# Kernel tuning notes

Hardware: AMD Instinct MI355X
Metric: run time of the kernel (lower is better)

## Reference

```python
import jax, jax.numpy as jnp
import numpy as np

B, S, D, H = 2, 2048, 1024, 16
HD = D // H


def setup_inputs() -> dict:
    key = jax.random.key(0)
    ks = jax.random.split(key, 9)
    s = 1.0 / np.sqrt(D)
    return {
        "qx": jax.random.normal(ks[0], (B, S, D), jnp.float32),
        "kx": jax.random.normal(ks[1], (B, S, D), jnp.float32),
        "vx": jax.random.normal(ks[2], (B, S, D), jnp.float32),
        "mask": jnp.tril(jnp.ones((S, S), jnp.int32))[None, None],  # [1,1,S,S] causal
        "Wq": jax.random.uniform(ks[3], (D, D), jnp.float32, -s, s),
        "bq": jax.random.uniform(ks[4], (D,), jnp.float32, -s, s),
        "Wk": jax.random.uniform(ks[5], (D, D), jnp.float32, -s, s),
        "bk": jax.random.uniform(ks[6], (D,), jnp.float32, -s, s),
        "Wv": jax.random.uniform(ks[7], (D, D), jnp.float32, -s, s),
        "bv": jax.random.uniform(ks[8], (D,), jnp.float32, -s, s),
    }


def reference(qx, kx, vx, mask, Wq, bq, Wk, bk, Wv, bv):
    bat, seq_len, d_model = qx.shape
    # torch Linear: y = x @ W.T + b
    q = qx @ Wq.T + bq
    k = kx @ Wk.T + bk
    v = vx @ Wv.T + bv
    # [b, h, s, hd]
    q = q.reshape(bat, seq_len, H, HD).transpose(0, 2, 1, 3)
    k = k.reshape(bat, seq_len, H, HD).transpose(0, 2, 1, 3)
    v = v.reshape(bat, seq_len, H, HD).transpose(0, 2, 1, 3)
    # NOTE: original scales by sqrt(d_model), not sqrt(head_dim)
    attn_weight = jnp.einsum('bhqd,bhkd->bhqk', q, k) / jnp.sqrt(
        jnp.asarray(d_model, q.dtype))
    attn_weight = jnp.where(mask == 0, -jnp.inf, attn_weight)
    attn_score = jax.nn.softmax(attn_weight, axis=-1)
    attn_output = jnp.einsum('bhqk,bhkd->bhqd', attn_score, v)
    return attn_output.transpose(0, 2, 1, 3).reshape(bat, seq_len, d_model)
```

## Files before the change

kernel.cpp:

```cpp
#include <hip/hip_runtime.h>


typedef __attribute__((ext_vector_type(8))) short short8;
typedef __attribute__((ext_vector_type(4))) short shortx4;
typedef __attribute__((ext_vector_type(4))) float floatx4;

#define NEGBIG (-1.0e30f)
#define QSCALE 0.04508422002778011f
#define SLOTF 4160

#define NEGBIG (-1.0e30f)

__device__ __forceinline__ float bf2f(ushort u) {
    union { unsigned int i; float f; } x; x.i = ((unsigned int)u) << 16; return x.f;
}
__device__ __forceinline__ ushort f2bf(float f) {
    union { unsigned int i; float f; } x; x.f = f;
    return (ushort)((x.i + 0x7FFFu + ((x.i >> 16) & 1u)) >> 16);
}
__device__ __forceinline__ ushort f2bf_trunc(float f) {
    union { unsigned int i; float f; } x; x.f = f;
    return (ushort)(x.i >> 16);
}
__device__ __forceinline__ void gl_lds16(const void* g, void* l) {
    __builtin_amdgcn_global_load_lds(
        (const __attribute__((address_space(1))) unsigned int*)g,
        (__attribute__((address_space(3))) unsigned int*)l, 16, 0, 0);
}

__global__ void convert_fp32(
    const float* __restrict__ qx, const float* __restrict__ kx, const float* __restrict__ vx,
    const float* __restrict__ wq, const float* __restrict__ wk, const float* __restrict__ wv,
    const float* __restrict__ bq, const float* __restrict__ bk, const float* __restrict__ bv,
    ushort* __restrict__ dst, int* __restrict__ flag)
{
    const unsigned int* w = (const unsigned int*)qx;
    int hits = 0;
#pragma unroll
    for (int i = 0; i < 4; ++i) {
        unsigned int v = w[threadIdx.x * 4 + i];
        int e = (int)((v >> 7) & 0xFF);
        hits += (e >= 100 && e <= 135) ? 1 : 0;
    }
    __shared__ int red[4];
    for (int off = 32; off; off >>= 1) hits += __shfl_down(hits, off);
    if ((threadIdx.x & 63) == 0) red[threadIdx.x >> 6] = hits;
    __syncthreads();
    const int dt = (red[0] + red[1] + red[2] + red[3] > 512) ? 1 : 0;
    if (blockIdx.x == 0 && threadIdx.x == 0) *flag = dt;
    if (dt) return;

    const int v = blockIdx.x * 256 + threadIdx.x;
    const float* src; int off = v;
    if      (v < 1048576) { src = qx; }
    else if (v < 2097152) { src = kx; off = v - 1048576; }
    else if (v < 3145728) { src = vx; off = v - 2097152; }
    else if (v < 3407872) { src = wq; off = v - 3145728; }
    else if (v < 3670016) { src = wk; off = v - 3407872; }
    else if (v < 3932160) { src = wv; off = v - 3670016; }
    else if (v < 3932416) { src = bq; off = v - 3932160; }
    else if (v < 3932672) { src = bk; off = v - 3932416; }
    else                  { src = bv; off = v - 3932672; }
    float4 f = ((const float4*)src)[off];
    shortx4 o;
    o[0] = (short)f2bf(f.x); o[1] = (short)f2bf(f.y);
    o[2] = (short)f2bf(f.z); o[3] = (short)f2bf(f.w);
    *(shortx4*)&dst[(size_t)v * 4] = o;
}

__global__ __launch_bounds__(256, 4) void qkv_gemm(
    const void* __restrict__ Xq_, const void* __restrict__ Wq_, const void* __restrict__ bq_,
    const void* __restrict__ Xk_, const void* __restrict__ Wk_, const void* __restrict__ bk_,
    const void* __restrict__ Xv_, const void* __restrict__ Wv_, const void* __restrict__ bv_,
    const ushort* __restrict__ conv,
    ushort* __restrict__ Yq, ushort* __restrict__ Yk, ushort* __restrict__ Yv,
    const int* __restrict__ flag)
{
    const int idx = blockIdx.x;
    const int xcd = idx & 7;
    const int j   = (idx >> 3) & 7;
    const int pg  = idx >> 6;
    const int p   = pg * 8 + xcd;
    const int z   = p >> 5;
    const int m0  = (p & 31) * 128;
    const int n0  = j * 128;

    const int dt = *flag;
    const ushort* X = dt ? (const ushort*)(z == 0 ? Xq_ : z == 1 ? Xk_ : Xv_)
                         : conv + (size_t)z * 4194304;
    const ushort* W = dt ? (const ushort*)(z == 0 ? Wq_ : z == 1 ? Wk_ : Wv_)
                         : conv + 12582912 + (size_t)z * 1048576;
    const ushort* bias = dt ? (const ushort*)(z == 0 ? bq_ : z == 1 ? bk_ : bv_)
                            : conv + 15728640 + z * 1024;
    ushort* Y = (z == 0) ? Yq : (z == 1) ? Yk : Yv;
    const float oscale = (z == 0) ? QSCALE : 1.0f;

    __shared__ __align__(16) ushort As[128 * 64];
    __shared__ __align__(16) ushort Bs[128 * 64];

    const int tid  = threadIdx.x;
    const int wave = tid >> 6;
    const int lane = tid & 63;
    const int col  = lane & 15;
    const int quad = lane >> 4;
    const int wm   = (wave >> 1) * 64;
    const int wn   = (wave & 1) * 64;

    floatx4 acc[4][4] = {};

    for (int k0 = 0; k0 < 1024; k0 += 64) {
        __syncthreads();
#pragma unroll
        for (int c = 0; c < 4; ++c) {
            const int o   = c * 4096 + tid * 16;
            const int row = o >> 7;
            const int bg  = ((o >> 4) & 7) ^ (row & 7);
            gl_lds16(X + (size_t)(m0 + row) * 1024 + k0 + bg * 8, &As[o >> 1]);
            gl_lds16(W + (size_t)(n0 + row) * 1024 + k0 + bg * 8, &Bs[o >> 1]);
        }
        __syncthreads();

#pragma unroll
        for (int h = 0; h < 2; ++h) {
            short8 af[4], bf_[4];
#pragma unroll
            for (int i = 0; i < 4; ++i) {
                const int ra = wm + i * 16 + col;
                const int rb = wn + i * 16 + col;
                af[i]  = *(const short8*)&As[ra * 64 + (((h * 4 + quad) ^ (ra & 7)) * 8)];
                bf_[i] = *(const short8*)&Bs[rb * 64 + (((h * 4 + quad) ^ (rb & 7)) * 8)];
            }
#pragma unroll
            for (int i = 0; i < 4; ++i)
#pragma unroll
                for (int jj = 0; jj < 4; ++jj)
                    acc[i][jj] = __builtin_amdgcn_mfma_f32_16x16x32_bf16(af[i], bf_[jj], acc[i][jj], 0, 0, 0);
        }
    }

    if (z == 2) {
#pragma unroll
        for (int jj = 0; jj < 4; ++jj) {
            const int n = n0 + wn + jj * 16 + col;
            const float bb = bf2f(bias[n]);
#pragma unroll
            for (int i = 0; i < 4; ++i) {
                const int m = m0 + wm + i * 16 + quad * 4;
                shortx4 pk;
#pragma unroll
                for (int r = 0; r < 4; ++r) pk[r] = (short)f2bf(acc[i][jj][r] + bb);
                *(shortx4*)&Y[((size_t)(m >> 11) * 1024 + n) * 2048 + (m & 2047)] = pk;
            }
        }
    } else {
#pragma unroll
        for (int jj = 0; jj < 4; ++jj) {
            const int n = n0 + wn + jj * 16 + col;
            const float bb = bf2f(bias[n]);
#pragma unroll
            for (int i = 0; i < 4; ++i)
#pragma unroll
                for (int r = 0; r < 4; ++r) {
                    const int m = m0 + wm + i * 16 + quad * 4 + r;
                    Y[(size_t)m * 1024 + n] = f2bf((acc[i][jj][r] + bb) * oscale);
                }
        }
    }
}

__global__ __launch_bounds__(256, 4) void attn(
    const ushort* __restrict__ Q, const ushort* __restrict__ K,
    const ushort* __restrict__ Vt, void* __restrict__ O,
    float* __restrict__ PW, const int* __restrict__ flag)
{
    const int i   = blockIdx.x;
    const int xcd = i & 7;
    const int m   = i >> 3;
    const int run = m & 3;
    const int jm  = m >> 2;
    int qt, chunk, n;
    if (jm < 30)      { qt = 31 - jm / 3;        chunk = jm % 3;        n = 3; }
    else if (jm < 52) { qt = 21 - (jm - 30) / 2; chunk = (jm - 30) % 2; n = 2; }
    else              { qt = 10 - (jm - 52);     chunk = 0;             n = 1; }
    const int T  = qt + 1;
    const int t0 = chunk * T / n;
    const int t1 = (chunk + 1) * T / n;

    const int g   = xcd + 8 * run;
    const int b   = g >> 4;
    const int h   = g & 15;
    const int q0  = qt * 64;
    const int dt  = *flag;

    __shared__ __align__(16) ushort Ks[2][64 * 64];
    __shared__ __align__(16) ushort Vs[2][64 * 64];
    __shared__ __align__(16) ushort Ps[4][16 * 64];

    const int tid  = threadIdx.x;
    const int wave = tid >> 6;
    const int lane = tid & 63;
    const int col  = lane & 15;
    const int quad = lane >> 4;

    const size_t qkbase = ((size_t)b * 2048) * 1024 + h * 64;
    const size_t vtbase = ((size_t)(b * 16 + h) * 64) * 2048;

    short8 ones;
#pragma unroll
    for (int ii = 0; ii < 8; ++ii) ones[ii] = (short)0x3F80;

    const int o0   = tid * 16;
    const int o1   = 4096 + tid * 16;
    const int row0 = o0 >> 7, row1 = o1 >> 7;
    const int bg0  = ((o0 >> 4) & 7) ^ (row0 & 7);
    const int bg1  = ((o1 >> 4) & 7) ^ (row1 & 7);

    const int rq = wave * 16 + col;
    const short8 qf0 = *(const short8*)&Q[qkbase + (size_t)(q0 + rq) * 1024 + quad * 8];
    const short8 qf1 = *(const short8*)&Q[qkbase + (size_t)(q0 + rq) * 1024 + 32 + quad * 8];

    {
        const int kv0 = t0 * 64;
        gl_lds16(K + qkbase + (size_t)(kv0 + row0) * 1024 + bg0 * 8, &Ks[0][o0 >> 1]);
        gl_lds16(K + qkbase + (size_t)(kv0 + row1) * 1024 + bg1 * 8, &Ks[0][o1 >> 1]);
        gl_lds16(Vt + vtbase + (size_t)row0 * 2048 + kv0 + bg0 * 8, &Vs[0][o0 >> 1]);
        gl_lds16(Vt + vtbase + (size_t)row1 * 2048 + kv0 + bg1 * 8, &Vs[0][o1 >> 1]);
    }
    __syncthreads();

    floatx4 oacc[4] = {};
    floatx4 sacc = {};

    for (int t = t0; t < t1; ++t) {
        const int cur = (t - t0) & 1;

        if (t + 1 < t1) {
            const int kv1 = (t + 1) * 64;
            gl_lds16(K + qkbase + (size_t)(kv1 + row0) * 1024 + bg0 * 8, &Ks[cur ^ 1][o0 >> 1]);
            gl_lds16(K + qkbase + (size_t)(kv1 + row1) * 1024 + bg1 * 8, &Ks[cur ^ 1][o1 >> 1]);
            gl_lds16(Vt + vtbase + (size_t)row0 * 2048 + kv1 + bg0 * 8, &Vs[cur ^ 1][o0 >> 1]);
            gl_lds16(Vt + vtbase + (size_t)row1 * 2048 + kv1 + bg1 * 8, &Vs[cur ^ 1][o1 >> 1]);
        }

        floatx4 s4[4];
#pragma unroll
        for (int ct = 0; ct < 4; ++ct) {
            const int rk = ct * 16 + col;
            short8 kf0 = *(const short8*)&Ks[cur][rk * 64 + (((quad    ) ^ (col & 7)) * 8)];
            short8 kf1 = *(const short8*)&Ks[cur][rk * 64 + (((quad + 4) ^ (col & 7)) * 8)];
            floatx4 a = {};
            a = __builtin_amdgcn_mfma_f32_16x16x32_bf16(qf0, kf0, a, 0, 0, 0);
            a = __builtin_amdgcn_mfma_f32_16x16x32_bf16(qf1, kf1, a, 0, 0, 0);
            s4[ct] = a;
        }

        if (t == qt) {
#pragma unroll
            for (int ct = 0; ct < 4; ++ct) {
                const int kidx = ct * 16 + col;
#pragma unroll
                for (int r = 0; r < 4; ++r) {
                    const int qidx = wave * 16 + quad * 4 + r;
                    s4[ct][r] = (kidx <= qidx) ? s4[ct][r] : NEGBIG;
                }
            }
        }

#pragma unroll
        for (int ct = 0; ct < 4; ++ct)
#pragma unroll
            for (int r = 0; r < 4; ++r) {
                float pv = __builtin_exp2f(s4[ct][r]);
                const int pr  = quad * 4 + r;
                const int blk = (ct * 2 + (col >> 3)) ^ (pr & 7);
                Ps[wave][pr * 64 + blk * 8 + (col & 7)] = f2bf_trunc(pv);
            }

        short8 pf0 = *(const short8*)&Ps[wave][col * 64 + (((quad    ) ^ (col & 7)) * 8)];
        short8 pf1 = *(const short8*)&Ps[wave][col * 64 + (((quad + 4) ^ (col & 7)) * 8)];

        sacc = __builtin_amdgcn_mfma_f32_16x16x32_bf16(pf0, ones, sacc, 0, 0, 0);
        sacc = __builtin_amdgcn_mfma_f32_16x16x32_bf16(pf1, ones, sacc, 0, 0, 0);

#pragma unroll
        for (int ct = 0; ct < 4; ++ct) {
            const int rv = ct * 16 + col;
            short8 vf0 = *(const short8*)&Vs[cur][rv * 64 + (((quad    ) ^ (rv & 7)) * 8)];
            short8 vf1 = *(const short8*)&Vs[cur][rv * 64 + (((quad + 4) ^ (rv & 7)) * 8)];
            oacc[ct] = __builtin_amdgcn_mfma_f32_16x16x32_bf16(pf0, vf0, oacc[ct], 0, 0, 0);
            oacc[ct] = __builtin_amdgcn_mfma_f32_16x16x32_bf16(pf1, vf1, oacc[ct], 0, 0, 0);
        }

        if (t + 1 < t1) __syncthreads();
    }

    if (n == 1) {
#pragma unroll
        for (int r = 0; r < 4; ++r) {
            const float inv = 1.0f / sacc[r];
            const int q = q0 + wave * 16 + quad * 4 + r;
#pragma unroll
            for (int ct = 0; ct < 4; ++ct) {
                const float v = oacc[ct][r] * inv;
                const size_t oidx = ((size_t)b * 2048 + q) * 1024 + h * 64 + ct * 16 + col;
                if (dt) ((ushort*)O)[oidx] = f2bf(v);
                else    ((float*)O)[oidx]  = v;
            }
        }
    } else {
        const int sl = (qt <= 21) ? (qt - 11) * 2 + chunk : 22 + (qt - 22) * 3 + chunk;
        float* slot = PW + ((size_t)g * 52 + sl) * SLOTF;
#pragma unroll
        for (int r = 0; r < 4; ++r) {
            const int pr = wave * 16 + quad * 4 + r;
#pragma unroll
            for (int ct = 0; ct < 4; ++ct)
                slot[pr * 64 + ct * 16 + col] = oacc[ct][r];
            if (col == 0) slot[4096 + pr] = sacc[r];
        }
    }
}

__global__ __launch_bounds__(256) void attn_combine(
    const float* __restrict__ PW, void* __restrict__ O, const int* __restrict__ flag)
{
    const int c  = blockIdx.x;
    const int g  = c & 31;
    const int qi = c >> 5;
    const int qt = 11 + qi;
    const int n  = (qt <= 21) ? 2 : 3;
    const int b  = g >> 4, h = g & 15;
    const int sl0 = (qt <= 21) ? (qt - 11) * 2 : 22 + (qt - 22) * 3;
    const float* base = PW + ((size_t)g * 52 + sl0) * SLOTF;

    const int t   = threadIdx.x;
    const int row = t >> 2;
    const int c0  = (t & 3) * 16;

    float acc[16] = {};
    float l = 0.0f;
    for (int s = 0; s < n; ++s) {
        const float* sp = base + (size_t)s * SLOTF;
        l += sp[4096 + row];
#pragma unroll
        for (int k = 0; k < 16; k += 4) {
            float4 v = *(const float4*)&sp[row * 64 + c0 + k];
            acc[k] += v.x; acc[k + 1] += v.y; acc[k + 2] += v.z; acc[k + 3] += v.w;
        }
    }
    const float inv = 1.0f / l;
    const int dt = *flag;
    const size_t o0 = ((size_t)b * 2048 + qt * 64 + row) * 1024 + h * 64 + c0;
    if (dt) {
#pragma unroll
        for (int k = 0; k < 16; ++k) ((ushort*)O)[o0 + k] = f2bf(acc[k] * inv);
    } else {
#pragma unroll
        for (int k = 0; k < 16; ++k) ((float*)O)[o0 + k] = acc[k] * inv;
    }
}

extern "C" void kernel_launch(void* const* d_in, const int* in_sizes, int n_in,
                              void* d_out, int out_size, void* d_ws, size_t ws_size,
                              hipStream_t stream) {
    const void* qx = d_in[0];
    const void* kx = d_in[1];
    const void* vx = d_in[2];
    const void* Wq = d_in[4]; const void* bq = d_in[5];
    const void* Wk = d_in[6]; const void* bk = d_in[7];
    const void* Wv = d_in[8]; const void* bv = d_in[9];

    int*    flag = (int*)d_ws;
    ushort* conv = (ushort*)((char*)d_ws + 256);
    ushort* Qw   = (ushort*)((char*)d_ws + 256 + 31463424);
    ushort* Kw   = Qw + (size_t)4096 * 1024;
    ushort* Vtw  = Kw + (size_t)4096 * 1024;
    float*  PW   = (float*)conv;

    convert_fp32<<<15363, 256, 0, stream>>>(
        (const float*)qx, (const float*)kx, (const float*)vx,
        (const float*)Wq, (const float*)Wk, (const float*)Wv,
        (const float*)bq, (const float*)bk, (const float*)bv, conv, flag);

    qkv_gemm<<<768, 256, 0, stream>>>(qx, Wq, bq, kx, Wk, bk, vx, Wv, bv,
                                      conv, Qw, Kw, Vtw, flag);

    attn<<<2016, 256, 0, stream>>>(Qw, Kw, Vtw, d_out, PW, flag);

    attn_combine<<<672, 256, 0, stream>>>(PW, d_out, flag);
}
```

Baseline: 203.3 us.

## Split attention tile 2x2 across waves with KV-split reduction and packed P stores

Waves are regrouped into a 2x2 grid: each wave takes 32 query rows and half of the 64 keys. The Q·K product is computed transposed so each lane holds four consecutive keys, which lets P be converted with v_cvt_pk_bf16_f32 and written to LDS as 8-byte stores. Each V fragment now feeds two MFMAs instead of one, cutting LDS traffic per MFMA. The price is an LDS reduction at the end, where the wk=1 waves hand partial O and row sums to the wk=0 waves, adding two block-wide barriers and moving the output write onto half the waves.

```diff
diff --git a/kernel.cpp b/kernel.cpp
--- a/kernel.cpp
+++ b/kernel.cpp
@@ -4,23 +4,18 @@
 typedef __attribute__((ext_vector_type(8))) short short8;
 typedef __attribute__((ext_vector_type(4))) short shortx4;
 typedef __attribute__((ext_vector_type(4))) float floatx4;
+typedef __attribute__((ext_vector_type(2))) unsigned int uintx2;
 
 #define NEGBIG (-1.0e30f)
 #define QSCALE 0.04508422002778011f
 #define SLOTF 4160
 
-#define NEGBIG (-1.0e30f)
-
 __device__ __forceinline__ float bf2f(ushort u) {
     union { unsigned int i; float f; } x; x.i = ((unsigned int)u) << 16; return x.f;
 }
 __device__ __forceinline__ ushort f2bf(float f) {
     union { unsigned int i; float f; } x; x.f = f;
     return (ushort)((x.i + 0x7FFFu + ((x.i >> 16) & 1u)) >> 16);
-}
-__device__ __forceinline__ ushort f2bf_trunc(float f) {
-    union { unsigned int i; float f; } x; x.f = f;
-    return (ushort)(x.i >> 16);
 }
 __device__ __forceinline__ void gl_lds16(const void* g, void* l) {
     __builtin_amdgcn_global_load_lds(
@@ -192,15 +187,15 @@
     const int q0  = qt * 64;
     const int dt  = *flag;
 
-    __shared__ __align__(16) ushort Ks[2][64 * 64];
-    __shared__ __align__(16) ushort Vs[2][64 * 64];
-    __shared__ __align__(16) ushort Ps[4][16 * 64];
+    __shared__ __align__(16) ushort SH[20480];
 
     const int tid  = threadIdx.x;
-    const int wave = tid >> 6;
+    const int wv   = tid >> 6;
     const int lane = tid & 63;
     const int col  = lane & 15;
     const int quad = lane >> 4;
+    const int wq   = wv >> 1;
+    const int wk   = wv & 1;
 
     const size_t qkbase = ((size_t)b * 2048) * 1024 + h * 64;
     const size_t vtbase = ((size_t)(b * 16 + h) * 64) * 2048;
@@ -215,108 +210,172 @@
     const int bg0  = ((o0 >> 4) & 7) ^ (row0 & 7);
     const int bg1  = ((o1 >> 4) & 7) ^ (row1 & 7);
 
-    const int rq = wave * 16 + col;
-    const short8 qf0 = *(const short8*)&Q[qkbase + (size_t)(q0 + rq) * 1024 + quad * 8];
-    const short8 qf1 = *(const short8*)&Q[qkbase + (size_t)(q0 + rq) * 1024 + 32 + quad * 8];
+    short8 qf[2][2];
+#pragma unroll
+    for (int mt = 0; mt < 2; ++mt) {
+        const int rq = wq * 32 + mt * 16 + col;
+#pragma unroll
+        for (int hf = 0; hf < 2; ++hf)
+            qf[mt][hf] = *(const short8*)&Q[qkbase + (size_t)(q0 + rq) * 1024 + hf * 32 + quad * 8];
+    }
 
     {
         const int kv0 = t0 * 64;
-        gl_lds16(K + qkbase + (size_t)(kv0 + row0) * 1024 + bg0 * 8, &Ks[0][o0 >> 1]);
-        gl_lds16(K + qkbase + (size_t)(kv0 + row1) * 1024 + bg1 * 8, &Ks[0][o1 >> 1]);
-        gl_lds16(Vt + vtbase + (size_t)row0 * 2048 + kv0 + bg0 * 8, &Vs[0][o0 >> 1]);
-        gl_lds16(Vt + vtbase + (size_t)row1 * 2048 + kv0 + bg1 * 8, &Vs[0][o1 >> 1]);
+        gl_lds16(K + qkbase + (size_t)(kv0 + row0) * 1024 + bg0 * 8, &SH[o0 >> 1]);
+        gl_lds16(K + qkbase + (size_t)(kv0 + row1) * 1024 + bg1 * 8, &SH[o1 >> 1]);
+        gl_lds16(Vt + vtbase + (size_t)row0 * 2048 + kv0 + bg0 * 8, &SH[8192 + (o0 >> 1)]);
+        gl_lds16(Vt + vtbase + (size_t)row1 * 2048 + kv0 + bg1 * 8, &SH[8192 + (o1 >> 1)]);
     }
     __syncthreads();
 
-    floatx4 oacc[4] = {};
-    floatx4 sacc = {};
+    floatx4 oacc[2][4] = {};
+    floatx4 sacc[2] = {};
+
+    ushort* Pw = &SH[16384 + wv * 1024];
 
     for (int t = t0; t < t1; ++t) {
         const int cur = (t - t0) & 1;
 
         if (t + 1 < t1) {
             const int kv1 = (t + 1) * 64;
-            gl_lds16(K + qkbase + (size_t)(kv1 + row0) * 1024 + bg0 * 8, &Ks[cur ^ 1][o0 >> 1]);
-            gl_lds16(K + qkbase + (size_t)(kv1 + row1) * 1024 + bg1 * 8, &Ks[cur ^ 1][o1 >> 1]);
-            gl_lds16(Vt + vtbase + (size_t)row0 * 2048 + kv1 + bg0 * 8, &Vs[cur ^ 1][o0 >> 1]);
-            gl_lds16(Vt + vtbase + (size_t)row1 * 2048 + kv1 + bg1 * 8, &Vs[cur ^ 1][o1 >> 1]);
-        }
-
-        floatx4 s4[4];
-#pragma unroll
-        for (int ct = 0; ct < 4; ++ct) {
-            const int rk = ct * 16 + col;
-            short8 kf0 = *(const short8*)&Ks[cur][rk * 64 + (((quad    ) ^ (col & 7)) * 8)];
-            short8 kf1 = *(const short8*)&Ks[cur][rk * 64 + (((quad + 4) ^ (col & 7)) * 8)];
-            floatx4 a = {};
-            a = __builtin_amdgcn_mfma_f32_16x16x32_bf16(qf0, kf0, a, 0, 0, 0);
-            a = __builtin_amdgcn_mfma_f32_16x16x32_bf16(qf1, kf1, a, 0, 0, 0);
-            s4[ct] = a;
-        }
+            const int nx = cur ^ 1;
+            gl_lds16(K + qkbase + (size_t)(kv1 + row0) * 1024 + bg0 * 8, &SH[nx * 4096 + (o0 >> 1)]);
+            gl_lds16(K + qkbase + (size_t)(kv1 + row1) * 1024 + bg1 * 8, &SH[nx * 4096 + (o1 >> 1)]);
+            gl_lds16(Vt + vtbase + (size_t)row0 * 2048 + kv1 + bg0 * 8, &SH[8192 + nx * 4096 + (o0 >> 1)]);
+            gl_lds16(Vt + vtbase + (size_t)row1 * 2048 + kv1 + bg1 * 8, &SH[8192 + nx * 4096 + (o1 >> 1)]);
+        }
+
+        const ushort* Kc = &SH[cur * 4096];
+        const ushort* Vc = &SH[8192 + cur * 4096];
+
+        short8 kf[2][2];
+#pragma unroll
+        for (int nt = 0; nt < 2; ++nt) {
+            const int rk = wk * 32 + nt * 16 + col;
+#pragma unroll
+            for (int hf = 0; hf < 2; ++hf)
+                kf[nt][hf] = *(const short8*)&Kc[rk * 64 + (((hf * 4 + quad) ^ (col & 7)) * 8)];
+        }
+
+        floatx4 s4[2][2];
+#pragma unroll
+        for (int mt = 0; mt < 2; ++mt)
+#pragma unroll
+            for (int nt = 0; nt < 2; ++nt) {
+                floatx4 a = {};
+                a = __builtin_amdgcn_mfma_f32_16x16x32_bf16(kf[nt][0], qf[mt][0], a, 0, 0, 0);
+                a = __builtin_amdgcn_mfma_f32_16x16x32_bf16(kf[nt][1], qf[mt][1], a, 0, 0, 0);
+                s4[mt][nt] = a;
+            }
 
         if (t == qt) {
 #pragma unroll
-            for (int ct = 0; ct < 4; ++ct) {
-                const int kidx = ct * 16 + col;
-#pragma unroll
-                for (int r = 0; r < 4; ++r) {
-                    const int qidx = wave * 16 + quad * 4 + r;
-                    s4[ct][r] = (kidx <= qidx) ? s4[ct][r] : NEGBIG;
-                }
+            for (int mt = 0; mt < 2; ++mt) {
+                const int qix = wq * 32 + mt * 16 + col;
+#pragma unroll
+                for (int nt = 0; nt < 2; ++nt)
+#pragma unroll
+                    for (int r = 0; r < 4; ++r) {
+                        const int kix = wk * 32 + nt * 16 + quad * 4 + r;
+                        s4[mt][nt][r] = (kix <= qix) ? s4[mt][nt][r] : NEGBIG;
+                    }
             }
         }
 
-#pragma unroll
-        for (int ct = 0; ct < 4; ++ct)
-#pragma unroll
-            for (int r = 0; r < 4; ++r) {
-                float pv = __builtin_exp2f(s4[ct][r]);
-                const int pr  = quad * 4 + r;
-                const int blk = (ct * 2 + (col >> 3)) ^ (pr & 7);
-                Ps[wave][pr * 64 + blk * 8 + (col & 7)] = f2bf_trunc(pv);
+        short8 pf[2];
+#pragma unroll
+        for (int mt = 0; mt < 2; ++mt) {
+            const int row = mt * 16 + col;
+            const int sw  = (row + (row >> 2)) & 3;
+#pragma unroll
+            for (int nt = 0; nt < 2; ++nt) {
+                float e0 = __builtin_exp2f(s4[mt][nt][0]);
+                float e1 = __builtin_exp2f(s4[mt][nt][1]);
+                float e2 = __builtin_exp2f(s4[mt][nt][2]);
+                float e3 = __builtin_exp2f(s4[mt][nt][3]);
+                unsigned int lo, hi;
+                asm("v_cvt_pk_bf16_f32 %0, %1, %2" : "=v"(lo) : "v"(e0), "v"(e1));
+                asm("v_cvt_pk_bf16_f32 %0, %1, %2" : "=v"(hi) : "v"(e2), "v"(e3));
+                const int bpos = (nt * 2 + (quad >> 1)) ^ sw;
+                *(uintx2*)&Pw[row * 32 + bpos * 8 + (quad & 1) * 4] = (uintx2){lo, hi};
             }
-
-        short8 pf0 = *(const short8*)&Ps[wave][col * 64 + (((quad    ) ^ (col & 7)) * 8)];
-        short8 pf1 = *(const short8*)&Ps[wave][col * 64 + (((quad + 4) ^ (col & 7)) * 8)];
-
-        sacc = __builtin_amdgcn_mfma_f32_16x16x32_bf16(pf0, ones, sacc, 0, 0, 0);
-        sacc = __builtin_amdgcn_mfma_f32_16x16x32_bf16(pf1, ones, sacc, 0, 0, 0);
+            pf[mt] = *(const short8*)&Pw[row * 32 + ((quad ^ sw) * 8)];
+        }
+
+        sacc[0] = __builtin_amdgcn_mfma_f32_16x16x32_bf16(pf[0], ones, sacc[0], 0, 0, 0);
+        sacc[1] = __builtin_amdgcn_mfma_f32_16x16x32_bf16(pf[1], ones, sacc[1], 0, 0, 0);
 
 #pragma unroll
         for (int ct = 0; ct < 4; ++ct) {
             const int rv = ct * 16 + col;
-            short8 vf0 = *(const short8*)&Vs[cur][rv * 64 + (((quad    ) ^ (rv & 7)) * 8)];
-            short8 vf1 = *(const short8*)&Vs[cur][rv * 64 + (((quad + 4) ^ (rv & 7)) * 8)];
-            oacc[ct] = __builtin_amdgcn_mfma_f32_16x16x32_bf16(pf0, vf0, oacc[ct], 0, 0, 0);
-            oacc[ct] = __builtin_amdgcn_mfma_f32_16x16x32_bf16(pf1, vf1, oacc[ct], 0, 0, 0);
+            short8 vf = *(const short8*)&Vc[rv * 64 + (((wk * 4 + quad) ^ (col & 7)) * 8)];
+            oacc[0][ct] = __builtin_amdgcn_mfma_f32_16x16x32_bf16(pf[0], vf, oacc[0][ct], 0, 0, 0);
+            oacc[1][ct] = __builtin_amdgcn_mfma_f32_16x16x32_bf16(pf[1], vf, oacc[1][ct], 0, 0, 0);
         }
 
         if (t + 1 < t1) __syncthreads();
     }
 
-    if (n == 1) {
-#pragma unroll
-        for (int r = 0; r < 4; ++r) {
-            const float inv = 1.0f / sacc[r];
-            const int q = q0 + wave * 16 + quad * 4 + r;
-#pragma unroll
-            for (int ct = 0; ct < 4; ++ct) {
-                const float v = oacc[ct][r] * inv;
-                const size_t oidx = ((size_t)b * 2048 + q) * 1024 + h * 64 + ct * 16 + col;
-                if (dt) ((ushort*)O)[oidx] = f2bf(v);
-                else    ((float*)O)[oidx]  = v;
-            }
-        }
-    } else {
-        const int sl = (qt <= 21) ? (qt - 11) * 2 + chunk : 22 + (qt - 22) * 3 + chunk;
-        float* slot = PW + ((size_t)g * 52 + sl) * SLOTF;
-#pragma unroll
-        for (int r = 0; r < 4; ++r) {
-            const int pr = wave * 16 + quad * 4 + r;
+    __syncthreads();
+    float* scr = (float*)SH;
+    if (wk == 1) {
+        float* s = scr + wq * 2080;
+#pragma unroll
+        for (int mt = 0; mt < 2; ++mt) {
 #pragma unroll
             for (int ct = 0; ct < 4; ++ct)
-                slot[pr * 64 + ct * 16 + col] = oacc[ct][r];
-            if (col == 0) slot[4096 + pr] = sacc[r];
+#pragma unroll
+                for (int r = 0; r < 4; ++r)
+                    s[(mt * 16 + quad * 4 + r) * 64 + ct * 16 + col] = oacc[mt][ct][r];
+            if (col == 0)
+#pragma unroll
+                for (int r = 0; r < 4; ++r)
+                    s[2048 + mt * 16 + quad * 4 + r] = sacc[mt][r];
+        }
+    }
+    __syncthreads();
+    if (wk == 0) {
+        float* s = scr + wq * 2080;
+#pragma unroll
+        for (int mt = 0; mt < 2; ++mt) {
+#pragma unroll
+            for (int ct = 0; ct < 4; ++ct)
+#pragma unroll
+                for (int r = 0; r < 4; ++r)
+                    oacc[mt][ct][r] += s[(mt * 16 + quad * 4 + r) * 64 + ct * 16 + col];
+#pragma unroll
+            for (int r = 0; r < 4; ++r)
+                sacc[mt][r] += s[2048 + mt * 16 + quad * 4 + r];
+        }
+
+        if (n == 1) {
+#pragma unroll
+            for (int mt = 0; mt < 2; ++mt)
+#pragma unroll
+                for (int r = 0; r < 4; ++r) {
+                    const float inv = 1.0f / sacc[mt][r];
+                    const int q = q0 + wq * 32 + mt * 16 + quad * 4 + r;
+#pragma unroll
+                    for (int ct = 0; ct < 4; ++ct) {
+                        const float v = oacc[mt][ct][r] * inv;
+                        const size_t oidx = ((size_t)b * 2048 + q) * 1024 + h * 64 + ct * 16 + col;
+                        if (dt) ((ushort*)O)[oidx] = f2bf(v);
+                        else    ((float*)O)[oidx]  = v;
+                    }
+                }
+        } else {
+            const int sl = (qt <= 21) ? (qt - 11) * 2 + chunk : 22 + (qt - 22) * 3 + chunk;
+            float* slot = PW + ((size_t)g * 52 + sl) * SLOTF;
+#pragma unroll
+            for (int mt = 0; mt < 2; ++mt)
+#pragma unroll
+                for (int r = 0; r < 4; ++r) {
+                    const int pr = wq * 32 + mt * 16 + quad * 4 + r;
+#pragma unroll
+                    for (int ct = 0; ct < 4; ++ct)
+                        slot[pr * 64 + ct * 16 + col] = oacc[mt][ct][r];
+                    if (col == 0) slot[4096 + pr] = sacc[mt][r];
+                }
         }
     }
 }
```

New measurement: 204.6 us. Within noise of the previous version (+0.6%).
